# Kernel tuning notes

Measured on AMD Instinct MI355X. Metric: run time of the kernel, lower is better.

Reference implementation:

```python
import jax, jax.numpy as jnp
import numpy as np

N = 100000
DEG = 16            # edges per source node (1 self-loop + 15 random)
E = N * DEG
IN_F = 128
OUT_F = 64
ALPHA = 0.2         # leaky relu negative slope


def _build_edges(key):
    # edges sorted by src (as adj.nonzero() would be), every node has >=1 out-edge
    src = jnp.repeat(jnp.arange(N, dtype=jnp.int32), DEG)
    dst = jax.random.randint(key, (E,), 0, N, dtype=jnp.int32)
    # force a self-loop as the first edge of every block
    self_pos = jnp.arange(E, dtype=jnp.int32) % DEG == 0
    dst = jnp.where(self_pos, src, dst)
    return jnp.stack([src, dst])  # [2, E]


def setup_inputs() -> dict:
    key = jax.random.key(0)
    k1, k2, k3, k4, k5, k6 = jax.random.split(key, 6)
    return {
        "input": jax.random.normal(k1, (N, IN_F), dtype=jnp.float32),
        "edge": _build_edges(k2),
        "W_high": jax.random.normal(k3, (IN_F, OUT_F), dtype=jnp.float32) * 0.1,
        "W_low": jax.random.normal(k4, (IN_F, OUT_F), dtype=jnp.float32) * 0.1,
        "a_high": jax.random.normal(k5, (1, 2 * OUT_F), dtype=jnp.float32) * 0.1,
        "a_low": jax.random.normal(k6, (1, 2 * OUT_F), dtype=jnp.float32) * 0.1,
    }


def _relu6(x):
    return jnp.clip(x, 0.0, 6.0)


def reference(input, edge, W_high, W_low, a_high, a_low):
    n = input.shape[0]
    src, dst = edge[0], edge[1]

    h_high = input @ W_high          # [N, F]
    h_low = input @ W_low            # [N, F]

    # a.mm(cat(h[src], h[dst]).T) == (h @ a_src)[src] + (h @ a_dst)[dst]
    f = W_high.shape[1]
    s_high = (h_high @ a_high[0, :f])[src] + (h_high @ a_high[0, f:])[dst]  # [E]
    s_low = (h_low @ a_low[0, :f])[src] + (h_low @ a_low[0, f:])[dst]

    edge_e_high = jnp.exp(-jax.nn.leaky_relu(s_high, ALPHA))  # [E], > 0
    edge_e_low = jnp.exp(-jax.nn.leaky_relu(s_low, ALPHA))

    seg = lambda v: jax.ops.segment_sum(v, src, num_segments=n, indices_are_sorted=True)

    # rowsum uses RAW exp values (before relu6/dropout), matching the source
    e_high_rowsum = seg(edge_e_high)[:, None]  # [N, 1]
    e_low_rowsum = seg(edge_e_low)[:, None]

    # relu6 clamp (dropout p=0 -> identity, eval mode)
    eh = _relu6(edge_e_high)
    el = _relu6(edge_e_low)

    # m @ (h[src] +/- h[dst]) == segment_sum over src of per-edge features
    h_agg_high = seg(h_high[src] + h_high[dst])   # [N, F]
    h_agg_low = seg(h_low[src] - h_low[dst])      # [N, F]

    # spmm: out[i] = sum_{(i,j)} e_ij * h_agg[j]
    h_prime_high = seg(eh[:, None] * h_agg_high[dst]) / e_high_rowsum
    h_prime_low = seg(el[:, None] * h_agg_low[dst]) / e_low_rowsum

    h_prime = 0.5 * (h_prime_high + h_prime_low)
    return _relu6(h_prime)  # concat=True
```

## Files before the change

### kernel.cpp

```cpp
#include <hip/hip_runtime.h>

#define N_NODES 100000
#define DEG 16
#define IN_F 128
#define OUT_F 64
#define E_EDGES (N_NODES * DEG)

typedef __bf16 bf16x8 __attribute__((ext_vector_type(8)));
typedef unsigned short u16x8 __attribute__((ext_vector_type(8)));
typedef float f32x4 __attribute__((ext_vector_type(4)));
typedef unsigned int u32x4 __attribute__((ext_vector_type(4)));

union BF8 { u16x8 u; bf16x8 b; };

__device__ inline float lo_bf(unsigned int u) {
    union { unsigned int i; float f; } v; v.i = u << 16; return v.f;
}
__device__ inline float hi_bf(unsigned int u) {
    union { unsigned int i; float f; } v; v.i = u & 0xFFFF0000u; return v.f;
}
__device__ inline unsigned short f2bf(float f) {
    union { float f; unsigned int i; } v; v.f = f;
    return (unsigned short)((v.i + 0x7FFFu + ((v.i >> 16) & 1u)) >> 16);
}
__device__ inline unsigned int packbf(float a, float b) {
    return (unsigned int)f2bf(a) | ((unsigned int)f2bf(b) << 16);
}

__global__ __launch_bounds__(256) void k_wprep(
    const float* __restrict__ Wh, const float* __restrict__ Wl,
    unsigned short* __restrict__ Wimg)
{
    int idx = blockIdx.x * 256 + threadIdx.x;
    int m = idx >> 13;
    int rem = idx & 8191;
    int k = rem >> 6, n = rem & 63;
    float v = m ? Wl[rem] : Wh[rem];
    Wimg[m * 8704 + n * 136 + k] = f2bf(v);
}

__global__ __launch_bounds__(256) void k_gemm(
    const float* __restrict__ in, const unsigned short* __restrict__ Wimg,
    unsigned int* __restrict__ H)
{
    __shared__ __align__(16) unsigned short ldsW[2][64][136];
    __shared__ __align__(16) unsigned short ldsA[64][136];

    {
        const u32x4* src = (const u32x4*)Wimg;
        u32x4* dst = (u32x4*)ldsW;
        for (int i = threadIdx.x; i < 2176; i += 256) dst[i] = src[i];
    }

    int row0B = blockIdx.x * 64;
    {
        const f32x4* src = (const f32x4*)(in + (size_t)row0B * IN_F);
        #pragma unroll
        for (int i = 0; i < 8; i++) {
            int c = threadIdx.x + 256 * i;
            int row = c >> 5;
            int kc = (c & 31) * 4;
            int grow = row0B + row;
            f32x4 v = (grow < N_NODES) ? src[c]
                      : *(const f32x4*)(in + (size_t)(N_NODES - 1) * IN_F + kc);
            unsigned int p0 = packbf(v[0], v[1]);
            unsigned int p1 = packbf(v[2], v[3]);
            *(unsigned int*)&ldsA[row][kc]     = p0;
            *(unsigned int*)&ldsA[row][kc + 2] = p1;
        }
    }
    __syncthreads();

    int wv = threadIdx.x >> 6;
    int lane = threadIdx.x & 63;
    int quad = lane >> 4, c = lane & 15;
    int row0 = row0B + wv * 16;

    bf16x8 afrag[4];
    #pragma unroll
    for (int kb = 0; kb < 4; kb++) {
        BF8 a;
        a.u = *(const u16x8*)&ldsA[wv * 16 + c][kb * 32 + quad * 8];
        afrag[kb] = a.b;
    }

    f32x4 acc[2][4];
    #pragma unroll
    for (int m = 0; m < 2; m++)
        #pragma unroll
        for (int t = 0; t < 4; t++) acc[m][t] = (f32x4){0, 0, 0, 0};

    #pragma unroll
    for (int kb = 0; kb < 4; kb++) {
        #pragma unroll
        for (int t = 0; t < 4; t++) {
            int n = t * 16 + c;
            BF8 bh, bl;
            bh.u = *(const u16x8*)&ldsW[0][n][kb * 32 + quad * 8];
            bl.u = *(const u16x8*)&ldsW[1][n][kb * 32 + quad * 8];
            acc[0][t] = __builtin_amdgcn_mfma_f32_16x16x32_bf16(afrag[kb], bh.b, acc[0][t], 0, 0, 0);
            acc[1][t] = __builtin_amdgcn_mfma_f32_16x16x32_bf16(afrag[kb], bl.b, acc[1][t], 0, 0, 0);
        }
    }

    #pragma unroll
    for (int r = 0; r < 4; r++) {
        int row = row0 + quad * 4 + r;
        if (row >= N_NODES) continue;
        size_t base = (size_t)row * OUT_F + c;
        #pragma unroll
        for (int t = 0; t < 4; t++)
            H[base + t * 16] = packbf(acc[0][t][r], acc[1][t][r]);
    }
}

__global__ __launch_bounds__(256) void k_agg(
    const unsigned int* __restrict__ H, const int* __restrict__ dst,
    const float* __restrict__ ah, const float* __restrict__ al,
    unsigned int* __restrict__ HAGG, f32x4* __restrict__ s)
{
    int lane = threadIdx.x & 63;
    int node = __builtin_amdgcn_readfirstlane(blockIdx.x * 4 + (threadIdx.x >> 6));
    const int* dp = dst + node * DEG;

    unsigned int hu = H[(size_t)node * 64 + lane];
    float hh = lo_bf(hu);
    float hl = hi_bf(hu);
    float sh = 16.0f * hh;
    float sl = 16.0f * hl;

    #pragma unroll
    for (int half = 0; half < 2; half++) {
        unsigned int u[8];
        #pragma unroll
        for (int t = 0; t < 8; t++) {
            int j = dp[half * 8 + t];
            u[t] = H[(size_t)j * 64 + lane];
        }
        #pragma unroll
        for (int t = 0; t < 8; t++) { sh += lo_bf(u[t]); sl -= hi_bf(u[t]); }
    }
    HAGG[(size_t)node * 64 + lane] = packbf(sh, sl);

    float ph = hh * ah[lane];
    float qh = hh * ah[64 + lane];
    float pl = hl * al[lane];
    float ql = hl * al[64 + lane];
    #pragma unroll
    for (int o = 32; o > 0; o >>= 1) {
        ph += __shfl_xor(ph, o);
        qh += __shfl_xor(qh, o);
        pl += __shfl_xor(pl, o);
        ql += __shfl_xor(ql, o);
    }
    if (lane == 0) s[node] = (f32x4){ph, qh, pl, ql};
}

__global__ __launch_bounds__(256) void k_out(
    const unsigned int* __restrict__ HAGG, const int* __restrict__ dst,
    const f32x4* __restrict__ s, float* __restrict__ out)
{
    int lane = threadIdx.x & 63;
    int node = __builtin_amdgcn_readfirstlane(blockIdx.x * 4 + (threadIdx.x >> 6));
    const int* dp = dst + node * DEG;

    int jl = dp[lane & 15];
    f32x4 si = s[node];
    f32x4 sj = s[jl];
    float xh = si.x + sj.y;
    float xl = si.z + sj.w;
    float lh = xh > 0.0f ? xh : 0.2f * xh;
    float ll = xl > 0.0f ? xl : 0.2f * xl;
    float wh = __expf(-lh);
    float wl = __expf(-ll);
    float rh = wh, rl = wl;
    #pragma unroll
    for (int o = 8; o > 0; o >>= 1) { rh += __shfl_xor(rh, o); rl += __shfl_xor(rl, o); }
    float eh = fminf(wh, 6.0f);
    float el = fminf(wl, 6.0f);

    float acc_h = 0.0f, acc_l = 0.0f;
    #pragma unroll
    for (int half = 0; half < 2; half++) {
        unsigned int u[8];
        float weh[8], wel[8];
        #pragma unroll
        for (int t = 0; t < 8; t++) {
            int j = dp[half * 8 + t];
            u[t] = HAGG[(size_t)j * 64 + lane];
        }
        #pragma unroll
        for (int t = 0; t < 8; t++) {
            weh[t] = __shfl(eh, half * 8 + t);
            wel[t] = __shfl(el, half * 8 + t);
        }
        #pragma unroll
        for (int t = 0; t < 8; t++) {
            acc_h += weh[t] * lo_bf(u[t]);
            acc_l += wel[t] * hi_bf(u[t]);
        }
    }
    float r = 0.5f * (acc_h / rh + acc_l / rl);
    r = fminf(fmaxf(r, 0.0f), 6.0f);
    out[(size_t)node * 64 + lane] = r;
}

extern "C" void kernel_launch(void* const* d_in, const int* in_sizes, int n_in,
                              void* d_out, int out_size, void* d_ws, size_t ws_size,
                              hipStream_t stream) {
    const float* input = (const float*)d_in[0];
    const int*   edge  = (const int*)d_in[1];
    const float* Wh    = (const float*)d_in[2];
    const float* Wl    = (const float*)d_in[3];
    const float* ah    = (const float*)d_in[4];
    const float* al    = (const float*)d_in[5];
    float* out = (float*)d_out;

    unsigned int* H    = (unsigned int*)d_ws;
    unsigned int* HAGG = H + (size_t)N_NODES * 64;
    f32x4* s = (f32x4*)(HAGG + (size_t)N_NODES * 64);
    unsigned short* Wimg = (unsigned short*)(s + N_NODES);

    const int* dstp = edge + E_EDGES;

    k_wprep<<<64, 256, 0, stream>>>(Wh, Wl, Wimg);
    k_gemm<<<1563, 256, 0, stream>>>(input, Wimg, H);
    k_agg<<<N_NODES / 4, 256, 0, stream>>>(H, dstp, ah, al, HAGG, s);
    k_out<<<N_NODES / 4, 256, 0, stream>>>(HAGG, dstp, s, out);
}
```

Before: 231.6 us.

## Split node features into column slices so each XCD gathers from an L2-resident slice

Stores the bf16-packed H and HAGG in 8 column-slice-major arrays of 8 u32 per node. The aggregation and output kernels derive the slice from blockIdx & 7, so under round-robin block dispatch each XCD gathers random neighbours from one 3.2MB slice that can stay in its L2, instead of from the full 25.6MB table. The attention score computation moves into its own k_s kernel, and a new k_edge kernel precomputes clamped edge weights and row sums into workspace that aliases the now-dead Hs region. In exchange there are two extra launches, extra round-trips through global memory for s, We and R, and 32-byte random reads that use only part of each cache line.

New measurement: 297.9 us. 28.6% more time.

```diff
diff --git a/kernel.cpp b/kernel.cpp
--- a/kernel.cpp
+++ b/kernel.cpp
@@ -5,10 +5,12 @@
 #define IN_F 128
 #define OUT_F 64
 #define E_EDGES (N_NODES * DEG)
+#define SLICE_U32 (N_NODES * 8)
 
 typedef __bf16 bf16x8 __attribute__((ext_vector_type(8)));
 typedef unsigned short u16x8 __attribute__((ext_vector_type(8)));
 typedef float f32x4 __attribute__((ext_vector_type(4)));
+typedef float f32x2 __attribute__((ext_vector_type(2)));
 typedef unsigned int u32x4 __attribute__((ext_vector_type(4)));
 
 union BF8 { u16x8 u; bf16x8 b; };
@@ -41,7 +43,7 @@
 
 __global__ __launch_bounds__(256) void k_gemm(
     const float* __restrict__ in, const unsigned short* __restrict__ Wimg,
-    unsigned int* __restrict__ H)
+    unsigned int* __restrict__ Hs)
 {
     __shared__ __align__(16) unsigned short ldsW[2][64][136];
     __shared__ __align__(16) unsigned short ldsA[64][136];
@@ -57,11 +59,11 @@
         const f32x4* src = (const f32x4*)(in + (size_t)row0B * IN_F);
         #pragma unroll
         for (int i = 0; i < 8; i++) {
-            int c = threadIdx.x + 256 * i;
-            int row = c >> 5;
-            int kc = (c & 31) * 4;
+            int cch = threadIdx.x + 256 * i;
+            int row = cch >> 5;
+            int kc = (cch & 31) * 4;
             int grow = row0B + row;
-            f32x4 v = (grow < N_NODES) ? src[c]
+            f32x4 v = (grow < N_NODES) ? src[cch]
                       : *(const f32x4*)(in + (size_t)(N_NODES - 1) * IN_F + kc);
             unsigned int p0 = packbf(v[0], v[1]);
             unsigned int p1 = packbf(v[2], v[3]);
@@ -107,41 +109,24 @@
     for (int r = 0; r < 4; r++) {
         int row = row0 + quad * 4 + r;
         if (row >= N_NODES) continue;
-        size_t base = (size_t)row * OUT_F + c;
-        #pragma unroll
-        for (int t = 0; t < 4; t++)
-            H[base + t * 16] = packbf(acc[0][t][r], acc[1][t][r]);
-    }
-}
-
-__global__ __launch_bounds__(256) void k_agg(
-    const unsigned int* __restrict__ H, const int* __restrict__ dst,
-    const float* __restrict__ ah, const float* __restrict__ al,
-    unsigned int* __restrict__ HAGG, f32x4* __restrict__ s)
+        #pragma unroll
+        for (int t = 0; t < 4; t++) {
+            int col = t * 16 + c;
+            Hs[(size_t)(col >> 3) * SLICE_U32 + (size_t)row * 8 + (col & 7)]
+                = packbf(acc[0][t][r], acc[1][t][r]);
+        }
+    }
+}
+
+__global__ __launch_bounds__(256) void k_s(
+    const unsigned int* __restrict__ Hs, const float* __restrict__ ah,
+    const float* __restrict__ al, f32x4* __restrict__ s)
 {
     int lane = threadIdx.x & 63;
     int node = __builtin_amdgcn_readfirstlane(blockIdx.x * 4 + (threadIdx.x >> 6));
-    const int* dp = dst + node * DEG;
-
-    unsigned int hu = H[(size_t)node * 64 + lane];
+    unsigned int hu = Hs[(size_t)(lane >> 3) * SLICE_U32 + (size_t)node * 8 + (lane & 7)];
     float hh = lo_bf(hu);
     float hl = hi_bf(hu);
-    float sh = 16.0f * hh;
-    float sl = 16.0f * hl;
-
-    #pragma unroll
-    for (int half = 0; half < 2; half++) {
-        unsigned int u[8];
-        #pragma unroll
-        for (int t = 0; t < 8; t++) {
-            int j = dp[half * 8 + t];
-            u[t] = H[(size_t)j * 64 + lane];
-        }
-        #pragma unroll
-        for (int t = 0; t < 8; t++) { sh += lo_bf(u[t]); sl -= hi_bf(u[t]); }
-    }
-    HAGG[(size_t)node * 64 + lane] = packbf(sh, sl);
-
     float ph = hh * ah[lane];
     float qh = hh * ah[64 + lane];
     float pl = hl * al[lane];
@@ -156,19 +141,48 @@
     if (lane == 0) s[node] = (f32x4){ph, qh, pl, ql};
 }
 
-__global__ __launch_bounds__(256) void k_out(
-    const unsigned int* __restrict__ HAGG, const int* __restrict__ dst,
-    const f32x4* __restrict__ s, float* __restrict__ out)
-{
-    int lane = threadIdx.x & 63;
-    int node = __builtin_amdgcn_readfirstlane(blockIdx.x * 4 + (threadIdx.x >> 6));
+__global__ __launch_bounds__(256) void k_aggh(
+    const unsigned int* __restrict__ Hs, const int* __restrict__ dst,
+    unsigned int* __restrict__ HAGGs)
+{
+    int slice = blockIdx.x & 7;
+    int nb = blockIdx.x >> 3;
+    int lane = threadIdx.x & 63;
+    int wid = threadIdx.x >> 6;
+    int c = lane & 7;
+    int node = nb * 32 + wid * 8 + (lane >> 3);
+    const unsigned int* base = Hs + (size_t)slice * SLICE_U32;
     const int* dp = dst + node * DEG;
 
-    int jl = dp[lane & 15];
-    f32x4 si = s[node];
-    f32x4 sj = s[jl];
-    float xh = si.x + sj.y;
-    float xl = si.z + sj.w;
+    unsigned int hu = base[(size_t)node * 8 + c];
+    float sh = 16.0f * lo_bf(hu);
+    float sl = 16.0f * hi_bf(hu);
+
+    #pragma unroll
+    for (int half = 0; half < 2; half++) {
+        unsigned int u[8];
+        #pragma unroll
+        for (int t = 0; t < 8; t++) {
+            int j = dp[half * 8 + t];
+            u[t] = base[(size_t)j * 8 + c];
+        }
+        #pragma unroll
+        for (int t = 0; t < 8; t++) { sh += lo_bf(u[t]); sl -= hi_bf(u[t]); }
+    }
+    HAGGs[(size_t)slice * SLICE_U32 + (size_t)node * 8 + c] = packbf(sh, sl);
+}
+
+__global__ __launch_bounds__(256) void k_edge(
+    const int* __restrict__ dst, const f32x4* __restrict__ s,
+    f32x2* __restrict__ We, f32x2* __restrict__ R)
+{
+    int g = blockIdx.x * 256 + threadIdx.x;
+    int i = g >> 4;
+    int j = dst[g];
+    f32x4 si = s[i];
+    f32x4 sj = s[j];
+    float xh = si[0] + sj[1];
+    float xl = si[2] + sj[3];
     float lh = xh > 0.0f ? xh : 0.2f * xh;
     float ll = xl > 0.0f ? xl : 0.2f * xl;
     float wh = __expf(-lh);
@@ -176,33 +190,49 @@
     float rh = wh, rl = wl;
     #pragma unroll
     for (int o = 8; o > 0; o >>= 1) { rh += __shfl_xor(rh, o); rl += __shfl_xor(rl, o); }
-    float eh = fminf(wh, 6.0f);
-    float el = fminf(wl, 6.0f);
+    We[g] = (f32x2){fminf(wh, 6.0f), fminf(wl, 6.0f)};
+    if ((g & 15) == 0) R[i] = (f32x2){rh, rl};
+}
+
+__global__ __launch_bounds__(256) void k_out(
+    const unsigned int* __restrict__ HAGGs, const int* __restrict__ dst,
+    const f32x2* __restrict__ We, const f32x2* __restrict__ R,
+    float* __restrict__ out)
+{
+    int slice = blockIdx.x & 7;
+    int nb = blockIdx.x >> 3;
+    int lane = threadIdx.x & 63;
+    int wid = threadIdx.x >> 6;
+    int c = lane & 7;
+    int node = nb * 32 + wid * 8 + (lane >> 3);
+    const unsigned int* base = HAGGs + (size_t)slice * SLICE_U32;
+    const int* dp = dst + node * DEG;
+    const f32x4* wp = (const f32x4*)(We + node * DEG);
+    f32x2 rr = R[node];
 
     float acc_h = 0.0f, acc_l = 0.0f;
     #pragma unroll
     for (int half = 0; half < 2; half++) {
         unsigned int u[8];
-        float weh[8], wel[8];
         #pragma unroll
         for (int t = 0; t < 8; t++) {
             int j = dp[half * 8 + t];
-            u[t] = HAGG[(size_t)j * 64 + lane];
-        }
-        #pragma unroll
-        for (int t = 0; t < 8; t++) {
-            weh[t] = __shfl(eh, half * 8 + t);
-            wel[t] = __shfl(el, half * 8 + t);
-        }
-        #pragma unroll
-        for (int t = 0; t < 8; t++) {
-            acc_h += weh[t] * lo_bf(u[t]);
-            acc_l += wel[t] * hi_bf(u[t]);
-        }
-    }
-    float r = 0.5f * (acc_h / rh + acc_l / rl);
+            u[t] = base[(size_t)j * 8 + c];
+        }
+        f32x4 w0 = wp[half * 4],     w1 = wp[half * 4 + 1];
+        f32x4 w2 = wp[half * 4 + 2], w3 = wp[half * 4 + 3];
+        acc_h += w0[0] * lo_bf(u[0]);  acc_l += w0[1] * hi_bf(u[0]);
+        acc_h += w0[2] * lo_bf(u[1]);  acc_l += w0[3] * hi_bf(u[1]);
+        acc_h += w1[0] * lo_bf(u[2]);  acc_l += w1[1] * hi_bf(u[2]);
+        acc_h += w1[2] * lo_bf(u[3]);  acc_l += w1[3] * hi_bf(u[3]);
+        acc_h += w2[0] * lo_bf(u[4]);  acc_l += w2[1] * hi_bf(u[4]);
+        acc_h += w2[2] * lo_bf(u[5]);  acc_l += w2[3] * hi_bf(u[5]);
+        acc_h += w3[0] * lo_bf(u[6]);  acc_l += w3[1] * hi_bf(u[6]);
+        acc_h += w3[2] * lo_bf(u[7]);  acc_l += w3[3] * hi_bf(u[7]);
+    }
+    float r = 0.5f * (acc_h / rr[0] + acc_l / rr[1]);
     r = fminf(fmaxf(r, 0.0f), 6.0f);
-    out[(size_t)node * 64 + lane] = r;
+    out[(size_t)node * OUT_F + slice * 8 + c] = r;
 }
 
 extern "C" void kernel_launch(void* const* d_in, const int* in_sizes, int n_in,
@@ -216,15 +246,19 @@
     const float* al    = (const float*)d_in[5];
     float* out = (float*)d_out;
 
-    unsigned int* H    = (unsigned int*)d_ws;
-    unsigned int* HAGG = H + (size_t)N_NODES * 64;
-    f32x4* s = (f32x4*)(HAGG + (size_t)N_NODES * 64);
+    unsigned int* Hs    = (unsigned int*)d_ws;
+    unsigned int* HAGGs = Hs + (size_t)8 * SLICE_U32;
+    f32x4* s = (f32x4*)(HAGGs + (size_t)8 * SLICE_U32);
     unsigned short* Wimg = (unsigned short*)(s + N_NODES);
+    f32x2* We = (f32x2*)d_ws;
+    f32x2* R  = (f32x2*)d_ws + E_EDGES;
 
     const int* dstp = edge + E_EDGES;
 
     k_wprep<<<64, 256, 0, stream>>>(Wh, Wl, Wimg);
-    k_gemm<<<1563, 256, 0, stream>>>(input, Wimg, H);
-    k_agg<<<N_NODES / 4, 256, 0, stream>>>(H, dstp, ah, al, HAGG, s);
-    k_out<<<N_NODES / 4, 256, 0, stream>>>(HAGG, dstp, s, out);
-}
+    k_gemm<<<1563, 256, 0, stream>>>(input, Wimg, Hs);
+    k_s<<<N_NODES / 4, 256, 0, stream>>>(Hs, ah, al, s);
+    k_aggh<<<25000, 256, 0, stream>>>(Hs, dstp, HAGGs);
+    k_edge<<<6250, 256, 0, stream>>>(dstp, s, We, R);
+    k_out<<<25000, 256, 0, stream>>>(HAGGs, dstp, We, R, out);
+}
```
